# Performance work log

Measured on AMD Instinct MI355X. Metric: run time of the kernel, lower is better.

The kernel has to match this reference:

```python
import jax, jax.numpy as jnp
import numpy as np

NUM_EMBEDDINGS = 512
EMBEDDING_DIM = 64
COMMITMENT_COST = 0.25


def setup_inputs() -> dict:
    key = jax.random.key(0)
    k1, k2 = jax.random.split(key)
    inputs = jax.random.normal(k1, (64, EMBEDDING_DIM, 32, 32), dtype=jnp.float32)
    # codebook initialized uniform(-1/K, 1/K) like the torch module
    bound = 1.0 / NUM_EMBEDDINGS
    embedding = jax.random.uniform(k2, (NUM_EMBEDDINGS, EMBEDDING_DIM),
                                   dtype=jnp.float32, minval=-bound, maxval=bound)
    return {"inputs": inputs, "embedding": embedding}


def reference(inputs, embedding):
    # NCHW -> NHWC
    x = jnp.transpose(inputs, (0, 2, 3, 1))
    B, H, W, D = x.shape
    K = embedding.shape[0]
    flat = x.reshape(-1, D)  # [N, D]
    # squared L2 distances to every codebook entry: [N, K]
    dist = (jnp.sum(flat * flat, axis=1, keepdims=True)
            + jnp.sum(embedding * embedding, axis=1)
            - 2.0 * flat @ embedding.T)
    idx = jnp.argmin(dist, axis=1)  # [N]
    # gather replaces one-hot @ codebook (same math)
    quantized = embedding[idx].reshape(B, H, W, D)
    e_latent_loss = jnp.mean((jax.lax.stop_gradient(quantized) - x) ** 2)
    q_latent_loss = jnp.mean((quantized - jax.lax.stop_gradient(x)) ** 2)
    loss = q_latent_loss + COMMITMENT_COST * e_latent_loss
    # straight-through estimator
    quantized_st = x + jax.lax.stop_gradient(quantized - x)
    # perplexity from code usage histogram (== mean of one-hot encodings)
    avg_probs = jnp.zeros((K,), dtype=x.dtype).at[idx].add(1.0) / idx.shape[0]
    perplexity = jnp.exp(-jnp.sum(avg_probs * jnp.log(avg_probs + 1e-10)))
    return (loss,
            jnp.transpose(quantized_st, (0, 3, 1, 2)),
            perplexity,
            quantized_st.reshape(B, -1))
```

## Files before the change

### kernel.cpp

```cpp
#include <hip/hip_runtime.h>


constexpr int DIM    = 64;
constexpr int KC     = 512;
constexpr int HW     = 1024;
constexpr int NPTS   = 65536;
constexpr int QELEMS = NPTS * DIM;

typedef float f32x16 __attribute__((ext_vector_type(16)));
typedef short bf16x8 __attribute__((ext_vector_type(8)));

__device__ inline unsigned short f2bf(float f) {
    unsigned u = __float_as_uint(f);
    u += 0x7FFF + ((u >> 16) & 1);
    return (unsigned short)(u >> 16);
}
__device__ inline float bf2f(unsigned short s) { return __uint_as_float(((unsigned)s) << 16); }

__device__ inline uint4 pack8(const unsigned short* s) {
    return make_uint4((unsigned)s[0] | ((unsigned)s[1] << 16),
                      (unsigned)s[2] | ((unsigned)s[3] << 16),
                      (unsigned)s[4] | ((unsigned)s[5] << 16),
                      (unsigned)s[6] | ((unsigned)s[7] << 16));
}

__global__ __launch_bounds__(256)
void vq_prep_kernel(const float* __restrict__ emb, unsigned short* __restrict__ EH)
{
    const int t = blockIdx.x * 256 + threadIdx.x;
    if (t < 4096) {
        const int c = t & 511, hb = t >> 9;
        const int d0 = 16 * (hb >> 1) + 4 * (hb & 1);
        const float* e = emb + (size_t)c * DIM;
        float4 v0 = *reinterpret_cast<const float4*>(e + d0);
        float4 v1 = *reinterpret_cast<const float4*>(e + d0 + 8);
        unsigned short s[8];
        s[0]=f2bf(-v0.x); s[1]=f2bf(-v0.y); s[2]=f2bf(-v0.z); s[3]=f2bf(-v0.w);
        s[4]=f2bf(-v1.x); s[5]=f2bf(-v1.y); s[6]=f2bf(-v1.z); s[7]=f2bf(-v1.w);
        *reinterpret_cast<uint4*>(EH + (size_t)(hb * KC + c) * 8) = pack8(s);
    } else if (t < 4608) {
        const int c = t - 4096;
        const float4* er = reinterpret_cast<const float4*>(emb + (size_t)c * DIM);
        float nrm = 0.f;
        #pragma unroll
        for (int i = 0; i < DIM / 4; ++i) {
            float4 v = er[i];
            nrm = fmaf(v.x,v.x,fmaf(v.y,v.y,fmaf(v.z,v.z,fmaf(v.w,v.w,nrm))));
        }
        float val = 0.5f + 0.5f * nrm;
        unsigned short nh = f2bf(val);
        unsigned short nl = f2bf(val - bf2f(nh));
        unsigned short ext[8] = {nh, nl, 0,0,0,0,0,0};
        unsigned short zer[8] = {0,0,0,0,0,0,0,0};
        *reinterpret_cast<uint4*>(EH + (size_t)(8 * KC + c) * 8) = pack8(ext);
        *reinterpret_cast<uint4*>(EH + (size_t)(9 * KC + c) * 8) = pack8(zer);
    }
}

__global__ __launch_bounds__(256, 4)
void vq_argmin_kernel(const float* __restrict__ x, const unsigned short* __restrict__ EH,
                      int* __restrict__ idx, int* __restrict__ hist,
                      float* __restrict__ loss_accum)
{
    __shared__ unsigned wkeys[4][32];

    const int tid  = threadIdx.x;
    const int w    = tid >> 6, lane = tid & 63;
    const int lo   = lane & 31, hi = lane >> 5;
    const int pair = w >> 1,  pw  = w & 1;

    const int n0  = blockIdx.x * 64 + pair * 32;
    const int b   = n0 >> 10;
    const int hw0 = n0 & (HW - 1);

    const float* xp = x + (size_t)b * (DIM * HW) + hw0 + lo;
    float xv[32];
    #pragma unroll
    for (int ks = 0; ks < 4; ++ks)
        #pragma unroll
        for (int j = 0; j < 8; ++j)
            xv[ks * 8 + j] = xp[(size_t)(16 * ks + 4 * hi + (j & 3) + 8 * (j >> 2)) * HW];

    bf16x8 BH[4], BL[4];
    float xnorm = 0.f;
    #pragma unroll
    for (int ks = 0; ks < 4; ++ks) {
        bf16x8 bh, bl;
        #pragma unroll
        for (int j = 0; j < 8; ++j) {
            float v = xv[ks * 8 + j];
            xnorm = fmaf(v, v, xnorm);
            unsigned short h = f2bf(v);
            bh[j] = (short)h;
            bl[j] = (short)f2bf(v - bf2f(h));
        }
        BH[ks] = bh; BL[ks] = bl;
    }
    bf16x8 B1 = {(short)0x3F80, (short)0x3F80, 0,0,0,0,0,0};

    unsigned rkey = 0xFFFFFFFFu;
    const int cbase = pw * 256;
    #pragma unroll
    for (int cc = 0; cc < 4; ++cc) {
        const int c0 = cbase + 64 * cc;
        bf16x8 A0[5], A1[5];
        #pragma unroll
        for (int ks = 0; ks < 4; ++ks) {
            const size_t base = (size_t)((2 * ks + hi) * KC + c0 + lo) * 8;
            A0[ks] = *reinterpret_cast<const bf16x8*>(EH + base);
            A1[ks] = *reinterpret_cast<const bf16x8*>(EH + base + 256);
        }
        {
            const size_t base = (size_t)((8 + hi) * KC + c0 + lo) * 8;
            A0[4] = *reinterpret_cast<const bf16x8*>(EH + base);
            A1[4] = *reinterpret_cast<const bf16x8*>(EH + base + 256);
        }
        f32x16 a0 = {}, a1 = {};
        #pragma unroll
        for (int ks = 0; ks < 4; ++ks) {
            a0 = __builtin_amdgcn_mfma_f32_32x32x16_bf16(A0[ks], BH[ks], a0, 0, 0, 0);
            a1 = __builtin_amdgcn_mfma_f32_32x32x16_bf16(A1[ks], BH[ks], a1, 0, 0, 0);
            a0 = __builtin_amdgcn_mfma_f32_32x32x16_bf16(A0[ks], BL[ks], a0, 0, 0, 0);
            a1 = __builtin_amdgcn_mfma_f32_32x32x16_bf16(A1[ks], BL[ks], a1, 0, 0, 0);
        }
        a0 = __builtin_amdgcn_mfma_f32_32x32x16_bf16(A0[4], B1, a0, 0, 0, 0);
        a1 = __builtin_amdgcn_mfma_f32_32x32x16_bf16(A1[4], B1, a1, 0, 0, 0);

        const unsigned kb0 = (unsigned)(c0 + 4 * hi), kb1 = kb0 + 32;
        unsigned m0 = 0xFFFFFFFFu, m1 = 0xFFFFFFFFu, m2 = 0xFFFFFFFFu, m3 = 0xFFFFFFFFu;
        #pragma unroll
        for (int r = 0; r < 16; ++r) {
            const unsigned kc = (unsigned)((r & 3) + 8 * (r >> 2));
            unsigned k0 = (__float_as_uint(a0[r]) & 0xFFFFFE00u) | (kb0 + kc);
            unsigned k1 = (__float_as_uint(a1[r]) & 0xFFFFFE00u) | (kb1 + kc);
            unsigned m  = min(k0, k1);
            if ((r & 3) == 0) m0 = min(m0, m);
            else if ((r & 3) == 1) m1 = min(m1, m);
            else if ((r & 3) == 2) m2 = min(m2, m);
            else m3 = min(m3, m);
        }
        rkey = min(rkey, min(min(m0, m1), min(m2, m3)));
    }

    rkey   = min(rkey, (unsigned)__shfl_xor((int)rkey, 32, 64));
    xnorm += __shfl_xor(xnorm, 32, 64);
    if (hi == 0) wkeys[w][lo] = rkey;
    __syncthreads();

    if (pw == 0) {
        const unsigned fkey = min(wkeys[2 * pair][lo], wkeys[2 * pair + 1][lo]);
        const int   code = (int)(fkey & 511u);
        const float v    = __uint_as_float(fkey & 0xFFFFFE00u);
        if (hi == 0) {
            idx[n0 + lo] = code;
            atomicAdd(&hist[code], 1);
        }
        float ls = (hi == 0) ? (2.f * v - 1.f + xnorm) : 0.f;
        #pragma unroll
        for (int off = 32; off > 0; off >>= 1) ls += __shfl_down(ls, off, 64);
        if (lane == 0) atomicAdd(loss_accum, ls);
    }
}

__global__ __launch_bounds__(256)
void vq_outputs_kernel(const float* __restrict__ emb, const int* __restrict__ idx,
                       float* __restrict__ out_nchw, float* __restrict__ out_flat)
{
    __shared__ float rows[64 * 65];
    __shared__ int   scode[64];

    const int tid = threadIdx.x;
    const int p0  = blockIdx.x * 64;
    const int b   = p0 >> 10;
    const int hw0 = p0 & (HW - 1);

    if (tid < 64) scode[tid] = idx[p0 + tid];
    __syncthreads();

    {
        const int p = tid >> 2, q = tid & 3;
        const float4* er = reinterpret_cast<const float4*>(emb + (size_t)scode[p] * DIM) + q * 4;
        float2* of = reinterpret_cast<float2*>(out_flat + (size_t)(p0 + p) * DIM + q * 16);
        float*  dst = &rows[p * 65 + q * 16];
        #pragma unroll
        for (int i = 0; i < 4; ++i) {
            float4 v = er[i];
            of[2 * i]     = make_float2(v.x, v.y);
            of[2 * i + 1] = make_float2(v.z, v.w);
            dst[4 * i + 0] = v.x; dst[4 * i + 1] = v.y;
            dst[4 * i + 2] = v.z; dst[4 * i + 3] = v.w;
        }
    }
    __syncthreads();
    {
        const int p = tid & 63, d0 = (tid >> 6) * 16;
        float* ob = out_nchw + (size_t)b * (DIM * HW) + hw0 + p;
        #pragma unroll
        for (int i = 0; i < 16; ++i)
            ob[(size_t)(d0 + i) * HW] = rows[p * 65 + d0 + i];
    }
}

__global__ __launch_bounds__(512, 1)
void vq_finalize_kernel(const int* __restrict__ hist, const float* __restrict__ loss_accum,
                        float* __restrict__ out_loss, float* __restrict__ out_perp)
{
    __shared__ float wsum[8];
    const int tid = threadIdx.x;
    const float p = (float)hist[tid] * (1.0f / (float)NPTS);
    float t = p * logf(p + 1e-10f);
    #pragma unroll
    for (int off = 32; off > 0; off >>= 1)
        t += __shfl_down(t, off, 64);
    if ((tid & 63) == 0) wsum[tid >> 6] = t;
    __syncthreads();
    if (tid == 0) {
        float s = 0.f;
        #pragma unroll
        for (int w = 0; w < 8; ++w) s += wsum[w];
        *out_perp = expf(-s);
        *out_loss = (*loss_accum) * 1.25f / (float)QELEMS;
    }
}

extern "C" void kernel_launch(void* const* d_in, const int* in_sizes, int n_in,
                              void* d_out, int out_size, void* d_ws, size_t ws_size,
                              hipStream_t stream)
{
    const float* x   = (const float*)d_in[0];
    const float* emb = (const float*)d_in[1];
    float* out = (float*)d_out;

    float*          loss_accum = (float*)d_ws;
    int*            hist       = (int*)((char*)d_ws + 64);
    unsigned short* EH         = (unsigned short*)((char*)d_ws + 4096);
    int*            idx        = (int*)((char*)d_ws + 4096 + 81920);

    hipMemsetAsync(d_ws, 0, 4096, stream);

    vq_prep_kernel<<<18, 256, 0, stream>>>(emb, EH);

    vq_argmin_kernel<<<NPTS / 64, 256, 0, stream>>>(x, EH, idx, hist, loss_accum);

    vq_outputs_kernel<<<NPTS / 64, 256, 0, stream>>>(emb, idx, out + 1, out + 2 + QELEMS);

    vq_finalize_kernel<<<1, 512, 0, stream>>>(hist, loss_accum, out, out + 1 + QELEMS);
}
```

Measured before the change: 133.4 us.

## Stage codebook fragments in LDS and give each wave the full codebook

The argmin kernel now copies the whole bf16 codebook fragment table (9 half-blocks, 72KB) into shared memory once per block. Each wave then scans all 512 codes for its own 32 points, instead of splitting codes across wave pairs and merging through LDS. This removes repeated global/L2 fragment loads and the cross-wave reduction. In exchange it costs a large LDS footprint that limits occupancy to about 2 blocks per CU, plus a per-block staging load. The memset is folded into the prep kernel and the unused zero half-block is dropped, with B1's high lanes zeroed to compensate.

```diff
diff --git a/kernel.cpp b/kernel.cpp
--- a/kernel.cpp
+++ b/kernel.cpp
@@ -6,6 +6,8 @@
 constexpr int HW     = 1024;
 constexpr int NPTS   = 65536;
 constexpr int QELEMS = NPTS * DIM;
+constexpr int NHB    = 9;
+constexpr int EHFRAG = NHB * KC;
 
 typedef float f32x16 __attribute__((ext_vector_type(16)));
 typedef short bf16x8 __attribute__((ext_vector_type(8)));
@@ -25,9 +27,13 @@
 }
 
 __global__ __launch_bounds__(256)
-void vq_prep_kernel(const float* __restrict__ emb, unsigned short* __restrict__ EH)
+void vq_prep_kernel(const float* __restrict__ emb, unsigned short* __restrict__ EH,
+                    int* __restrict__ hist, float* __restrict__ loss_accum)
 {
     const int t = blockIdx.x * 256 + threadIdx.x;
+    if (t < 512) hist[t] = 0;
+    if (t == 512) *loss_accum = 0.f;
+
     if (t < 4096) {
         const int c = t & 511, hb = t >> 9;
         const int d0 = 16 * (hb >> 1) + 4 * (hb & 1);
@@ -51,25 +57,22 @@
         unsigned short nh = f2bf(val);
         unsigned short nl = f2bf(val - bf2f(nh));
         unsigned short ext[8] = {nh, nl, 0,0,0,0,0,0};
-        unsigned short zer[8] = {0,0,0,0,0,0,0,0};
         *reinterpret_cast<uint4*>(EH + (size_t)(8 * KC + c) * 8) = pack8(ext);
-        *reinterpret_cast<uint4*>(EH + (size_t)(9 * KC + c) * 8) = pack8(zer);
-    }
-}
-
-__global__ __launch_bounds__(256, 4)
-void vq_argmin_kernel(const float* __restrict__ x, const unsigned short* __restrict__ EH,
+    }
+}
+
+__global__ __launch_bounds__(256, 2)
+void vq_argmin_kernel(const float* __restrict__ x, const uint4* __restrict__ EHg,
                       int* __restrict__ idx, int* __restrict__ hist,
                       float* __restrict__ loss_accum)
 {
-    __shared__ unsigned wkeys[4][32];
+    __shared__ uint4 sEH[EHFRAG];
 
     const int tid  = threadIdx.x;
     const int w    = tid >> 6, lane = tid & 63;
     const int lo   = lane & 31, hi = lane >> 5;
-    const int pair = w >> 1,  pw  = w & 1;
-
-    const int n0  = blockIdx.x * 64 + pair * 32;
+
+    const int n0  = blockIdx.x * 128 + w * 32;
     const int b   = n0 >> 10;
     const int hw0 = n0 & (HW - 1);
 
@@ -80,6 +83,9 @@
         #pragma unroll
         for (int j = 0; j < 8; ++j)
             xv[ks * 8 + j] = xp[(size_t)(16 * ks + 4 * hi + (j & 3) + 8 * (j >> 2)) * HW];
+
+    for (int i = tid; i < EHFRAG; i += 256)
+        sEH[i] = EHg[i];
 
     bf16x8 BH[4], BL[4];
     float xnorm = 0.f;
@@ -96,36 +102,32 @@
         }
         BH[ks] = bh; BL[ks] = bl;
     }
-    bf16x8 B1 = {(short)0x3F80, (short)0x3F80, 0,0,0,0,0,0};
+    bf16x8 B1 = {};
+    if (hi == 0) { B1[0] = (short)0x3F80; B1[1] = (short)0x3F80; }
+
+    __syncthreads();
+    const bf16x8* sA = reinterpret_cast<const bf16x8*>(sEH);
 
     unsigned rkey = 0xFFFFFFFFu;
-    const int cbase = pw * 256;
-    #pragma unroll
-    for (int cc = 0; cc < 4; ++cc) {
-        const int c0 = cbase + 64 * cc;
-        bf16x8 A0[5], A1[5];
+    #pragma unroll
+    for (int cc = 0; cc < 8; ++cc) {
+        const int c0 = 64 * cc;
+        f32x16 a0 = {}, a1 = {};
         #pragma unroll
         for (int ks = 0; ks < 4; ++ks) {
-            const size_t base = (size_t)((2 * ks + hi) * KC + c0 + lo) * 8;
-            A0[ks] = *reinterpret_cast<const bf16x8*>(EH + base);
-            A1[ks] = *reinterpret_cast<const bf16x8*>(EH + base + 256);
+            bf16x8 A0 = sA[(2 * ks + hi) * KC + c0 + lo];
+            bf16x8 A1 = sA[(2 * ks + hi) * KC + c0 + 32 + lo];
+            a0 = __builtin_amdgcn_mfma_f32_32x32x16_bf16(A0, BH[ks], a0, 0, 0, 0);
+            a1 = __builtin_amdgcn_mfma_f32_32x32x16_bf16(A1, BH[ks], a1, 0, 0, 0);
+            a0 = __builtin_amdgcn_mfma_f32_32x32x16_bf16(A0, BL[ks], a0, 0, 0, 0);
+            a1 = __builtin_amdgcn_mfma_f32_32x32x16_bf16(A1, BL[ks], a1, 0, 0, 0);
         }
         {
-            const size_t base = (size_t)((8 + hi) * KC + c0 + lo) * 8;
-            A0[4] = *reinterpret_cast<const bf16x8*>(EH + base);
-            A1[4] = *reinterpret_cast<const bf16x8*>(EH + base + 256);
-        }
-        f32x16 a0 = {}, a1 = {};
-        #pragma unroll
-        for (int ks = 0; ks < 4; ++ks) {
-            a0 = __builtin_amdgcn_mfma_f32_32x32x16_bf16(A0[ks], BH[ks], a0, 0, 0, 0);
-            a1 = __builtin_amdgcn_mfma_f32_32x32x16_bf16(A1[ks], BH[ks], a1, 0, 0, 0);
-            a0 = __builtin_amdgcn_mfma_f32_32x32x16_bf16(A0[ks], BL[ks], a0, 0, 0, 0);
-            a1 = __builtin_amdgcn_mfma_f32_32x32x16_bf16(A1[ks], BL[ks], a1, 0, 0, 0);
-        }
-        a0 = __builtin_amdgcn_mfma_f32_32x32x16_bf16(A0[4], B1, a0, 0, 0, 0);
-        a1 = __builtin_amdgcn_mfma_f32_32x32x16_bf16(A1[4], B1, a1, 0, 0, 0);
-
+            bf16x8 N0 = sA[8 * KC + c0 + lo];
+            bf16x8 N1 = sA[8 * KC + c0 + 32 + lo];
+            a0 = __builtin_amdgcn_mfma_f32_32x32x16_bf16(N0, B1, a0, 0, 0, 0);
+            a1 = __builtin_amdgcn_mfma_f32_32x32x16_bf16(N1, B1, a1, 0, 0, 0);
+        }
         const unsigned kb0 = (unsigned)(c0 + 4 * hi), kb1 = kb0 + 32;
         unsigned m0 = 0xFFFFFFFFu, m1 = 0xFFFFFFFFu, m2 = 0xFFFFFFFFu, m3 = 0xFFFFFFFFu;
         #pragma unroll
@@ -144,22 +146,17 @@
 
     rkey   = min(rkey, (unsigned)__shfl_xor((int)rkey, 32, 64));
     xnorm += __shfl_xor(xnorm, 32, 64);
-    if (hi == 0) wkeys[w][lo] = rkey;
-    __syncthreads();
-
-    if (pw == 0) {
-        const unsigned fkey = min(wkeys[2 * pair][lo], wkeys[2 * pair + 1][lo]);
-        const int   code = (int)(fkey & 511u);
-        const float v    = __uint_as_float(fkey & 0xFFFFFE00u);
-        if (hi == 0) {
-            idx[n0 + lo] = code;
-            atomicAdd(&hist[code], 1);
-        }
-        float ls = (hi == 0) ? (2.f * v - 1.f + xnorm) : 0.f;
-        #pragma unroll
-        for (int off = 32; off > 0; off >>= 1) ls += __shfl_down(ls, off, 64);
-        if (lane == 0) atomicAdd(loss_accum, ls);
-    }
+
+    const int   code = (int)(rkey & 511u);
+    const float v    = __uint_as_float(rkey & 0xFFFFFE00u);
+    if (hi == 0) {
+        idx[n0 + lo] = code;
+        atomicAdd(&hist[code], 1);
+    }
+    float ls = (hi == 0) ? (2.f * v - 1.f + xnorm) : 0.f;
+    #pragma unroll
+    for (int off = 32; off > 0; off >>= 1) ls += __shfl_down(ls, off, 64);
+    if (lane == 0) atomicAdd(loss_accum, ls);
 }
 
 __global__ __launch_bounds__(256)
@@ -234,13 +231,11 @@
     float*          loss_accum = (float*)d_ws;
     int*            hist       = (int*)((char*)d_ws + 64);
     unsigned short* EH         = (unsigned short*)((char*)d_ws + 4096);
-    int*            idx        = (int*)((char*)d_ws + 4096 + 81920);
-
-    hipMemsetAsync(d_ws, 0, 4096, stream);
-
-    vq_prep_kernel<<<18, 256, 0, stream>>>(emb, EH);
-
-    vq_argmin_kernel<<<NPTS / 64, 256, 0, stream>>>(x, EH, idx, hist, loss_accum);
+    int*            idx        = (int*)((char*)d_ws + 4096 + 73728);
+
+    vq_prep_kernel<<<18, 256, 0, stream>>>(emb, EH, hist, loss_accum);
+
+    vq_argmin_kernel<<<NPTS / 128, 256, 0, stream>>>(x, (const uint4*)EH, idx, hist, loss_accum);
 
     vq_outputs_kernel<<<NPTS / 64, 256, 0, stream>>>(emb, idx, out + 1, out + 2 + QELEMS);
 
```

After: 130.5 us. 1.02x faster.

## Fuse argmin and output gather into one kernel, drop memset and idx buffer

Applied to the files above, without the earlier changes.

Merges the argmin kernel and the output-writing kernel, so each block writes the NCHW and flat outputs right after finding its codes, with the work split between the two wave halves. This removes the idx round trip through global memory, one kernel launch, and the hipMemsetAsync, whose zeroing now happens inside the prep kernel. The norm extension row is read from a single row, with B1 masked per half-wave instead of a zero row. The code-block loop is no longer unrolled and launch bounds are relaxed to 2 blocks per CU, which changes register pressure and occupancy. The NCHW writes now come straight from registers with strided stores instead of an LDS transpose.

```diff
diff --git a/kernel.cpp b/kernel.cpp
--- a/kernel.cpp
+++ b/kernel.cpp
@@ -25,9 +25,13 @@
 }
 
 __global__ __launch_bounds__(256)
-void vq_prep_kernel(const float* __restrict__ emb, unsigned short* __restrict__ EH)
+void vq_prep_kernel(const float* __restrict__ emb, unsigned short* __restrict__ EH,
+                    int* __restrict__ hist, float* __restrict__ loss_accum)
 {
     const int t = blockIdx.x * 256 + threadIdx.x;
+    if (t < 512) hist[t] = 0;
+    if (t == 512) *loss_accum = 0.f;
+
     if (t < 4096) {
         const int c = t & 511, hb = t >> 9;
         const int d0 = 16 * (hb >> 1) + 4 * (hb & 1);
@@ -51,16 +55,15 @@
         unsigned short nh = f2bf(val);
         unsigned short nl = f2bf(val - bf2f(nh));
         unsigned short ext[8] = {nh, nl, 0,0,0,0,0,0};
-        unsigned short zer[8] = {0,0,0,0,0,0,0,0};
         *reinterpret_cast<uint4*>(EH + (size_t)(8 * KC + c) * 8) = pack8(ext);
-        *reinterpret_cast<uint4*>(EH + (size_t)(9 * KC + c) * 8) = pack8(zer);
-    }
-}
-
-__global__ __launch_bounds__(256, 4)
-void vq_argmin_kernel(const float* __restrict__ x, const unsigned short* __restrict__ EH,
-                      int* __restrict__ idx, int* __restrict__ hist,
-                      float* __restrict__ loss_accum)
+    }
+}
+
+__global__ __launch_bounds__(256, 2) __attribute__((amdgpu_waves_per_eu(2, 4)))
+void vq_main_kernel(const float* __restrict__ x, const float* __restrict__ emb,
+                    const unsigned short* __restrict__ EH,
+                    int* __restrict__ hist, float* __restrict__ loss_accum,
+                    float* __restrict__ out_nchw, float* __restrict__ out_flat)
 {
     __shared__ unsigned wkeys[4][32];
 
@@ -96,11 +99,11 @@
         }
         BH[ks] = bh; BL[ks] = bl;
     }
-    bf16x8 B1 = {(short)0x3F80, (short)0x3F80, 0,0,0,0,0,0};
+    bf16x8 B1 = {};
+    if (hi == 0) { B1[0] = (short)0x3F80; B1[1] = (short)0x3F80; }
 
     unsigned rkey = 0xFFFFFFFFu;
     const int cbase = pw * 256;
-    #pragma unroll
     for (int cc = 0; cc < 4; ++cc) {
         const int c0 = cbase + 64 * cc;
         bf16x8 A0[5], A1[5];
@@ -111,7 +114,7 @@
             A1[ks] = *reinterpret_cast<const bf16x8*>(EH + base + 256);
         }
         {
-            const size_t base = (size_t)((8 + hi) * KC + c0 + lo) * 8;
+            const size_t base = (size_t)(8 * KC + c0 + lo) * 8;
             A0[4] = *reinterpret_cast<const bf16x8*>(EH + base);
             A1[4] = *reinterpret_cast<const bf16x8*>(EH + base + 256);
         }
@@ -146,58 +149,44 @@
     xnorm += __shfl_xor(xnorm, 32, 64);
     if (hi == 0) wkeys[w][lo] = rkey;
     __syncthreads();
+    const unsigned fkey = min(wkeys[2 * pair][lo], wkeys[2 * pair + 1][lo]);
 
     if (pw == 0) {
-        const unsigned fkey = min(wkeys[2 * pair][lo], wkeys[2 * pair + 1][lo]);
-        const int   code = (int)(fkey & 511u);
-        const float v    = __uint_as_float(fkey & 0xFFFFFE00u);
-        if (hi == 0) {
-            idx[n0 + lo] = code;
-            atomicAdd(&hist[code], 1);
-        }
-        float ls = (hi == 0) ? (2.f * v - 1.f + xnorm) : 0.f;
-        #pragma unroll
-        for (int off = 32; off > 0; off >>= 1) ls += __shfl_down(ls, off, 64);
-        if (lane == 0) atomicAdd(loss_accum, ls);
-    }
-}
-
-__global__ __launch_bounds__(256)
-void vq_outputs_kernel(const float* __restrict__ emb, const int* __restrict__ idx,
-                       float* __restrict__ out_nchw, float* __restrict__ out_flat)
-{
-    __shared__ float rows[64 * 65];
-    __shared__ int   scode[64];
-
-    const int tid = threadIdx.x;
-    const int p0  = blockIdx.x * 64;
-    const int b   = p0 >> 10;
-    const int hw0 = p0 & (HW - 1);
-
-    if (tid < 64) scode[tid] = idx[p0 + tid];
-    __syncthreads();
-
-    {
-        const int p = tid >> 2, q = tid & 3;
-        const float4* er = reinterpret_cast<const float4*>(emb + (size_t)scode[p] * DIM) + q * 4;
-        float2* of = reinterpret_cast<float2*>(out_flat + (size_t)(p0 + p) * DIM + q * 16);
-        float*  dst = &rows[p * 65 + q * 16];
-        #pragma unroll
-        for (int i = 0; i < 4; ++i) {
-            float4 v = er[i];
-            of[2 * i]     = make_float2(v.x, v.y);
-            of[2 * i + 1] = make_float2(v.z, v.w);
-            dst[4 * i + 0] = v.x; dst[4 * i + 1] = v.y;
-            dst[4 * i + 2] = v.z; dst[4 * i + 3] = v.w;
-        }
-    }
-    __syncthreads();
-    {
-        const int p = tid & 63, d0 = (tid >> 6) * 16;
+        {
+            const int   code = (int)(fkey & 511u);
+            const float v    = __uint_as_float(fkey & 0xFFFFFE00u);
+            if (hi == 0) atomicAdd(&hist[code], 1);
+            float ls = (hi == 0) ? (2.f * v - 1.f + xnorm) : 0.f;
+            #pragma unroll
+            for (int off = 32; off > 0; off >>= 1) ls += __shfl_down(ls, off, 64);
+            if (lane == 0) atomicAdd(loss_accum, ls);
+        }
+        const int p = lane >> 1, q = lane & 1;
+        const int code = __shfl((int)fkey, p, 64) & 511;
+        const float4* er = reinterpret_cast<const float4*>(emb + (size_t)code * DIM) + q * 8;
+        float4 vv[8];
+        #pragma unroll
+        for (int j = 0; j < 8; ++j) vv[j] = er[j];
         float* ob = out_nchw + (size_t)b * (DIM * HW) + hw0 + p;
         #pragma unroll
+        for (int j = 0; j < 8; ++j) {
+            const int d = q * 32 + 4 * j;
+            ob[(size_t)(d + 0) * HW] = vv[j].x;
+            ob[(size_t)(d + 1) * HW] = vv[j].y;
+            ob[(size_t)(d + 2) * HW] = vv[j].z;
+            ob[(size_t)(d + 3) * HW] = vv[j].w;
+        }
+    } else {
+        int    codes[16];
+        #pragma unroll
+        for (int i = 0; i < 16; ++i) codes[i] = __shfl((int)fkey, 2 * i + hi, 64) & 511;
+        float2 vv[16];
+        #pragma unroll
         for (int i = 0; i < 16; ++i)
-            ob[(size_t)(d0 + i) * HW] = rows[p * 65 + d0 + i];
+            vv[i] = *reinterpret_cast<const float2*>(emb + (size_t)codes[i] * DIM + 2 * lo);
+        #pragma unroll
+        for (int i = 0; i < 16; ++i)
+            *reinterpret_cast<float2*>(out_flat + (size_t)(n0 + 2 * i + hi) * DIM + 2 * lo) = vv[i];
     }
 }
 
@@ -234,15 +223,11 @@
     float*          loss_accum = (float*)d_ws;
     int*            hist       = (int*)((char*)d_ws + 64);
     unsigned short* EH         = (unsigned short*)((char*)d_ws + 4096);
-    int*            idx        = (int*)((char*)d_ws + 4096 + 81920);
-
-    hipMemsetAsync(d_ws, 0, 4096, stream);
-
-    vq_prep_kernel<<<18, 256, 0, stream>>>(emb, EH);
-
-    vq_argmin_kernel<<<NPTS / 64, 256, 0, stream>>>(x, EH, idx, hist, loss_accum);
-
-    vq_outputs_kernel<<<NPTS / 64, 256, 0, stream>>>(emb, idx, out + 1, out + 2 + QELEMS);
+
+    vq_prep_kernel<<<18, 256, 0, stream>>>(emb, EH, hist, loss_accum);
+
+    vq_main_kernel<<<NPTS / 64, 256, 0, stream>>>(x, emb, EH, hist, loss_accum,
+                                                  out + 1, out + 2 + QELEMS);
 
     vq_finalize_kernel<<<1, 512, 0, stream>>>(hist, loss_accum, out, out + 1 + QELEMS);
 }
```

New measurement: 129.2 us. 3.2% less time.
